# Kernel optimization log

Hardware: AMD Instinct MI355X
Metric: run time of the kernel (lower is better)

Reference implementation:

```python
import jax, jax.numpy as jnp
import numpy as np

B, H, D = 4096, 64, 32
HID, KS, K = 256, 5, 4
RES_L1_W, ENT_W, BAL_W, SPACE_W = 0.05, 0.01, 0.1, 0.1
TARGET_PROBS = jnp.array([0.5, 0.5], dtype=jnp.float32)
MIN_SPACING_RATIO = 0.5
EPS = 1e-8


def gelu(x):
    return jax.nn.gelu(x, approximate=False)  # torch nn.GELU default (exact)


def conv1d(x, w, b):
    # x: (B, Cin, H), w: (Cout, Cin, KS) -> (B, Cout, H), 'same' padding
    pad = w.shape[-1] // 2
    y = jax.lax.conv_general_dilated(
        x, w, window_strides=(1,), padding=[(pad, pad)],
        dimension_numbers=("NCH", "OIH", "NCH"))
    return y + b[None, :, None]


def _pw_linear_interp(pos, vals):
    # pos: (B, K) sorted anchor positions in [0, H-1]; vals: (B, K, D)
    t = jnp.arange(H, dtype=pos.dtype)                    # (H,)
    # index of left anchor for each timestep (searchsorted-right, K is tiny)
    idx = jnp.sum(pos[:, None, :] <= t[None, :, None], axis=-1) - 1  # (B, H)
    idx = jnp.clip(idx, 0, K - 2)
    left = jnp.take_along_axis(pos, idx, axis=1)          # (B, H)
    right = jnp.take_along_axis(pos, idx + 1, axis=1)     # (B, H)
    w = jnp.clip((t[None, :] - left) / (right - left + EPS), 0.0, 1.0)
    vl = jnp.take_along_axis(vals, idx[..., None], axis=1)        # (B, H, D)
    vr = jnp.take_along_axis(vals, (idx + 1)[..., None], axis=1)  # (B, H, D)
    return vl + w[..., None] * (vr - vl)


def setup_inputs() -> dict:
    key = jax.random.key(0)
    ks = jax.random.split(key, 24)
    s = 0.02
    inp = {
        "action_chunk": jax.random.normal(ks[0], (B, H, D), jnp.float32),
        "conv_w0": jax.random.normal(ks[1], (HID, D, KS), jnp.float32) * s,
        "conv_b0": jnp.zeros((HID,), jnp.float32),
        "conv_w1": jax.random.normal(ks[2], (HID, HID, KS), jnp.float32) * s,
        "conv_b1": jnp.zeros((HID,), jnp.float32),
        "conv_w2": jax.random.normal(ks[3], (HID, HID, KS), jnp.float32) * s,
        "conv_b2": jnp.zeros((HID,), jnp.float32),
        "proj_w": jax.random.normal(ks[4], (HID, HID), jnp.float32) * s,
        "proj_b": jnp.zeros((HID,), jnp.float32),
        "val_w1": jax.random.normal(ks[5], (HID, HID), jnp.float32) * s,
        "val_b1": jnp.zeros((HID,), jnp.float32),
        "val_w2": jax.random.normal(ks[6], (HID, K * D), jnp.float32) * s,
        "val_b2": jnp.zeros((K * D,), jnp.float32),
        "pos_w1": jax.random.normal(ks[7], (HID, HID), jnp.float32) * s,
        "pos_b1": jnp.zeros((HID,), jnp.float32),
        "pos_w2": jax.random.normal(ks[8], (HID, K), jnp.float32) * s,
        "pos_b2": jnp.zeros((K,), jnp.float32),
        "res_w1": jax.random.normal(ks[9], (HID, HID), jnp.float32) * s,
        "res_b1": jnp.zeros((HID,), jnp.float32),
        "res_w2": jax.random.normal(ks[10], (HID, H * D), jnp.float32) * s,
        "res_b2": jnp.zeros((H * D,), jnp.float32),
        "mix_w": jax.random.normal(ks[11], (HID, 2), jnp.float32) * s,
        "mix_b": jnp.zeros((2,), jnp.float32),
    }
    return inp


def reference(action_chunk, conv_w0, conv_b0, conv_w1, conv_b1, conv_w2, conv_b2,
              proj_w, proj_b, val_w1, val_b1, val_w2, val_b2,
              pos_w1, pos_b1, pos_w2, pos_b2,
              res_w1, res_b1, res_w2, res_b2, mix_w, mix_b):
    # --- temporal encoder (eval mode: dropout identity) ---
    x = jnp.swapaxes(action_chunk, 1, 2)                  # (B, D, H)
    h = gelu(conv1d(x, conv_w0, conv_b0))
    h = gelu(conv1d(h, conv_w1, conv_b1))
    h = gelu(conv1d(h, conv_w2, conv_b2))                 # (B, HID, H)
    pooled = h.mean(axis=-1)                              # adaptive avg pool -> (B, HID)
    enc = gelu(pooled @ proj_w + proj_b)                  # (B, HID)

    # --- coarse anchor decoder ---
    anchor_vals = (gelu(enc @ val_w1 + val_b1) @ val_w2 + val_b2).reshape(B, K, D)
    raw_pos = gelu(enc @ pos_w1 + pos_b1) @ pos_w2 + pos_b2          # (B, K)
    scaled = jax.nn.sigmoid(raw_pos) * float(H - 1)
    order = jnp.argsort(scaled, axis=-1)
    pos = jnp.take_along_axis(scaled, order, axis=-1)
    pos = pos.at[:, 0].set(0.0).at[:, -1].set(float(H - 1))
    vals = jnp.take_along_axis(anchor_vals, order[..., None], axis=1)
    coarse = _pw_linear_interp(pos, vals)                 # (B, H, D)

    # --- residual correction ---
    residual = (gelu(enc @ res_w1 + res_b1) @ res_w2 + res_b2).reshape(B, H, D)
    fine = coarse + residual

    # --- mixture routing (global/local) ---
    q = jax.nn.softmax(enc @ mix_w + mix_b, axis=-1)      # (B, 2)
    recon = q[:, 0, None, None] * coarse + q[:, 1, None, None] * fine

    # --- losses (fusable elementwise+reduction chain) ---
    recon_loss = jnp.mean((recon - action_chunk) ** 2)
    l1 = jnp.mean(jnp.abs(residual))
    ent = -jnp.mean(jnp.sum(q * jnp.log(q + EPS), axis=-1))
    mean_q = q.mean(axis=0)
    balance = jnp.sum((mean_q - TARGET_PROBS) ** 2)
    gaps = pos[:, 1:] - pos[:, :-1]
    min_gap = MIN_SPACING_RATIO * float(H - 1) / float(K - 1)
    spacing = jnp.mean(jnp.mean(jax.nn.relu(min_gap - gaps) ** 2, axis=-1))
    total = recon_loss + RES_L1_W * l1 + ENT_W * ent + BAL_W * balance + SPACE_W * spacing
    return total
```

## Files before the change

kernel.cpp:

```cpp
#include <hip/hip_runtime.h>

#define NB 4096

typedef __attribute__((ext_vector_type(8)))  __bf16 bf16x8;
typedef __attribute__((ext_vector_type(4)))  float  f32x4;
typedef __attribute__((ext_vector_type(16))) float  f32x16;
typedef __attribute__((ext_vector_type(8)))  int    i32x8;
typedef __attribute__((ext_vector_type(4)))  int    i32x4;

__device__ __forceinline__ float gelu_fast(float x){
    float x2 = x * x;
    float z  = x * (-1.59576912f - 0.07135482f * x2);
    float e  = __expf(z);
    return x * __builtin_amdgcn_rcpf(1.0f + e);
}
__device__ __forceinline__ unsigned short f2bf(float x){
    unsigned b = __float_as_uint(x);
    b += 0x7fffu + ((b >> 16) & 1u);
    return (unsigned short)(b >> 16);
}
__device__ __forceinline__ unsigned char f2fp8(float x){
    int p = __builtin_amdgcn_cvt_pk_fp8_f32(x, x, 0, false);
    return (unsigned char)(p & 0xff);
}
__device__ __forceinline__ unsigned f2fp4(float x){
    unsigned s = (__float_as_uint(x) >> 31) & 1u;
    float m = fabsf(x);
    int c;
    if      (m < 0.25f) c = 0;
    else if (m < 0.75f) c = 1;
    else if (m < 1.25f) c = 2;
    else if (m < 1.75f) c = 3;
    else if (m < 2.5f)  c = 4;
    else if (m < 3.5f)  c = 5;
    else if (m < 5.0f)  c = 6;
    else                c = 7;
    return (s << 3) | (unsigned)c;
}

#define O_WP0  0
#define O_WP1  40960
#define O_WP2  368640
#define O_PROJ 696320
#define O_VAL1 761856
#define O_POS1 827392
#define O_RES1 892928
#define O_VAL2 958464
#define O_RES2 991232
#define O_POS2 1515520
#define O_MIX  1519616
#define PK_TOTAL 1523712

#define WQ4_BYTES 163840

__device__ __forceinline__ unsigned short pack_std_elem(const float* W, int N, int t){
    int j = t & 7, lane = (t >> 3) & 63, rest = t >> 9;
    int ntcnt = N >> 4;
    int nt = rest % ntcnt, kk = rest / ntcnt;
    int n = nt*16 + (lane & 15), k = kk*32 + ((lane >> 4) << 3) + j;
    return f2bf(W[k * N + n]);
}
__device__ __forceinline__ unsigned short pack_pad_elem(const float* W, int Nreal, int t){
    int j = t & 7, lane = (t >> 3) & 63, kk = t >> 9;
    int n = lane & 15, k = kk*32 + ((lane >> 4) << 3) + j;
    return (n < Nreal) ? f2bf(W[k * Nreal + n]) : (unsigned short)0;
}
__device__ __forceinline__ unsigned char pack_fp4_byte(const float* W, int t){
    int byt = t & 15, lane = (t >> 4) & 63, g = (t >> 10) & 7, S = t >> 13;
    int n = g*32 + (lane & 31);
    int kbase = S*64 + ((lane >> 5) << 5) + (byt << 1);
    int k0 = kbase, k1 = kbase + 1;
    float v0 = W[n*1280 + (k0 & 255)*5 + (k0 >> 8)] * 64.0f;
    float v1 = W[n*1280 + (k1 & 255)*5 + (k1 >> 8)] * 64.0f;
    return (unsigned char)(f2fp4(v0) | (f2fp4(v1) << 4));
}

__global__ __launch_bounds__(256) void pack_weights(
    const float* __restrict__ W0, const float* __restrict__ W1, const float* __restrict__ W2,
    const float* __restrict__ proj_w, const float* __restrict__ val_w1,
    const float* __restrict__ pos_w1, const float* __restrict__ res_w1,
    const float* __restrict__ val_w2, const float* __restrict__ res_w2,
    const float* __restrict__ pos_w2, const float* __restrict__ mix_w,
    unsigned short* __restrict__ pk,
    unsigned char* __restrict__ wq1, unsigned char* __restrict__ wq2)
{
    int idx = blockIdx.x * 256 + threadIdx.x;
    if (idx >= PK_TOTAL) return;
    if (idx < O_WP1){
        int t = idx;
        int j = t & 7, lane = (t >> 3) & 63, nt = (t >> 9) & 7, s = t >> 12;
        int co = nt*32 + (lane & 31);
        int tap = s >> 1, ci = ((s & 1) << 4) + ((lane >> 5) << 3) + j;
        pk[idx] = f2bf(W0[co*160 + ci*5 + tap]);
    } else if (idx < O_WP1 + WQ4_BYTES){
        wq1[idx - O_WP1] = pack_fp4_byte(W1, idx - O_WP1);
    } else if (idx < O_WP2){
    } else if (idx < O_WP2 + WQ4_BYTES){
        wq2[idx - O_WP2] = pack_fp4_byte(W2, idx - O_WP2);
    } else if (idx < O_PROJ){
    }
    else if (idx < O_VAL1) pk[idx] = pack_std_elem(proj_w, 256, idx - O_PROJ);
    else if (idx < O_POS1) pk[idx] = pack_std_elem(val_w1, 256, idx - O_VAL1);
    else if (idx < O_RES1) pk[idx] = pack_std_elem(pos_w1, 256, idx - O_POS1);
    else if (idx < O_VAL2) pk[idx] = pack_std_elem(res_w1, 256, idx - O_RES1);
    else if (idx < O_RES2) pk[idx] = pack_std_elem(val_w2, 128, idx - O_VAL2);
    else if (idx < O_POS2) pk[idx] = pack_std_elem(res_w2, 2048, idx - O_RES2);
    else if (idx < O_MIX)  pk[idx] = pack_pad_elem(pos_w2, 4, idx - O_POS2);
    else                   pk[idx] = pack_pad_elem(mix_w, 2, idx - O_MIX);
}

#define HT_P 272
#define XT_S 40
#define INV512 0.001953125f
#define SCALE1 0x7F

__global__ __launch_bounds__(256, 4) void conv_mfma_kernel(
    const float* __restrict__ A,
    const float* __restrict__ B0, const float* __restrict__ B1, const float* __restrict__ B2,
    const unsigned short* __restrict__ wp0,
    const unsigned char* __restrict__ wq1, const unsigned char* __restrict__ wq2,
    unsigned short* __restrict__ pooled)
{
    __shared__ __align__(16) unsigned short xt[68 * XT_S];
    __shared__ __align__(16) unsigned char  ht8[68 * HT_P];

    const int tid  = threadIdx.x;
    const int b    = blockIdx.x;
    const int w    = tid >> 6;
    const int lane = tid & 63;
    const int l31  = lane & 31;
    const int hi   = lane >> 5;
    const int hi8  = hi << 3;
    const int w64  = w << 6;

    for (int i = tid; i < 4 * HT_P; i += 256){
        int r = i / HT_P, c = i - r * HT_P;
        int rr = (r < 2 ? r : r + 64);
        ht8[rr * HT_P + c] = 0;
    }
    if (tid < 128){
        int r = tid >> 5, c = tid & 31;
        int rr = (r < 2 ? r : r + 64);
        xt[rr * XT_S + c] = 0;
    }
    {
        const float* Ab = A + (size_t)b * 2048;
        int e0 = tid << 3;
        int t = e0 >> 5, c = e0 & 31;
        const float4* p = (const float4*)(Ab + e0);
        float4 v0 = p[0], v1 = p[1];
        union { unsigned short u[8]; bf16x8 v; } pkv;
        pkv.u[0]=f2bf(v0.x); pkv.u[1]=f2bf(v0.y); pkv.u[2]=f2bf(v0.z); pkv.u[3]=f2bf(v0.w);
        pkv.u[4]=f2bf(v1.x); pkv.u[5]=f2bf(v1.y); pkv.u[6]=f2bf(v1.z); pkv.u[7]=f2bf(v1.w);
        *(bf16x8*)&xt[(t + 2) * XT_S + c] = pkv.v;
    }
    __syncthreads();

    f32x16 acc[2][2];

#define ZEROALL \
    { _Pragma("unroll") for (int mt = 0; mt < 2; ++mt) \
      _Pragma("unroll") for (int nn = 0; nn < 2; ++nn) \
      _Pragma("unroll") for (int r = 0; r < 16; ++r) acc[mt][nn][r] = 0.f; }

#define LOADAX(BUF, S) \
    { _Pragma("unroll") for (int mt = 0; mt < 2; ++mt) \
          BUF[mt] = *(const bf16x8*)&xt[((mt << 5) + l31 + ((S) >> 1)) * XT_S + (((S) & 1) << 4) + hi8]; }
#define LOADB0(BUF, S) \
    { _Pragma("unroll") for (int nn = 0; nn < 2; ++nn) \
          BUF[nn] = *(const bf16x8*)(b0ptr + nn * 512 + (S) * 4096); }
#define MFX(X_, B_) \
    { _Pragma("unroll") for (int mt = 0; mt < 2; ++mt) \
      _Pragma("unroll") for (int nn = 0; nn < 2; ++nn) \
          acc[mt][nn] = __builtin_amdgcn_mfma_f32_32x32x16_bf16(X_[mt], B_[nn], acc[mt][nn], 0, 0, 0); }

#define LOADA_MX(DST, S) \
    { _Pragma("unroll") for (int mt = 0; mt < 2; ++mt) \
          DST[mt] = *(const i32x8*)&ht8[((mt << 5) + l31 + ((S) >> 2)) * HT_P + (((S) & 3) << 6) + (hi << 5)]; }
#define LOADB4(DST, S, BPTR) \
    { _Pragma("unroll") for (int nn = 0; nn < 2; ++nn) \
          *(i32x4*)&DST[nn] = *(const i32x4*)((BPTR) + (size_t)(S) * 8192 + nn * 1024); }
#define MFMX4(A_, B_) \
    { _Pragma("unroll") for (int mt = 0; mt < 2; ++mt) \
      _Pragma("unroll") for (int nn = 0; nn < 2; ++nn) \
          acc[mt][nn] = __builtin_amdgcn_mfma_scale_f32_32x32x64_f8f6f4( \
              A_[mt], B_[nn], acc[mt][nn], 0, 4, 0, SCALE1, 0, SCALE1); }

#define EPI_C0(BIAS) \
    { float bvn[2]; \
      _Pragma("unroll") for (int nn = 0; nn < 2; ++nn) bvn[nn] = (BIAS)[w64 + (nn << 5) + l31]; \
      _Pragma("unroll") for (int mt = 0; mt < 2; ++mt) \
      _Pragma("unroll") for (int nn = 0; nn < 2; ++nn) \
      _Pragma("unroll") for (int r = 0; r < 16; ++r){ \
          int row = (mt << 5) + (r & 3) + ((r >> 2) << 3) + (hi << 2) + 2; \
          float v = gelu_fast(acc[mt][nn][r] + bvn[nn]); \
          ht8[row * HT_P + w64 + (nn << 5) + l31] = f2fp8(v * 8.0f); } }

#define EPI_MX(BIAS) \
    { float bvn[2]; \
      _Pragma("unroll") for (int nn = 0; nn < 2; ++nn) bvn[nn] = (BIAS)[w64 + (nn << 5) + l31]; \
      _Pragma("unroll") for (int mt = 0; mt < 2; ++mt) \
      _Pragma("unroll") for (int nn = 0; nn < 2; ++nn) \
      _Pragma("unroll") for (int r = 0; r < 16; ++r){ \
          int row = (mt << 5) + (r & 3) + ((r >> 2) << 3) + (hi << 2) + 2; \
          float v = gelu_fast(acc[mt][nn][r] * INV512 + bvn[nn]); \
          ht8[row * HT_P + w64 + (nn << 5) + l31] = f2fp8(v * 8.0f); } }

#define CONV_MX4(WQ) \
    { const unsigned char* bptr = (WQ) + (size_t)((w << 11) + lane * 16); \
      i32x8 Bf[2][2]; i32x8 Af[2][2]; \
      _Pragma("unroll") for (int rr_ = 0; rr_ < 2; ++rr_) \
      _Pragma("unroll") for (int nn = 0; nn < 2; ++nn) \
      _Pragma("unroll") for (int e_ = 0; e_ < 8; ++e_) Bf[rr_][nn][e_] = 0; \
      LOADB4(Bf[0], 0, bptr); LOADA_MX(Af[0], 0); \
      LOADB4(Bf[1], 1, bptr); LOADA_MX(Af[1], 1); \
      _Pragma("unroll") \
      for (int s = 0; s < 20; ++s){ \
          MFMX4(Af[s & 1], Bf[s & 1]); \
          if (s + 2 < 20){ LOADB4(Bf[s & 1], s + 2, bptr); LOADA_MX(Af[s & 1], s + 2); } \
      } }

    ZEROALL;
    {
        const unsigned short* b0ptr = wp0 + (size_t)((w << 10) + lane * 8);
        bf16x8 Bc[2][2]; bf16x8 Xc[2][2];
        LOADB0(Bc[0], 0); LOADAX(Xc[0], 0);
        LOADB0(Bc[1], 1); LOADAX(Xc[1], 1);
        #pragma unroll
        for (int s = 0; s < 10; ++s){
            MFX(Xc[s & 1], Bc[s & 1]);
            if (s + 2 < 10){ LOADB0(Bc[s & 1], s + 2); LOADAX(Xc[s & 1], s + 2); }
        }
    }
    EPI_C0(B0);
    __syncthreads();

    ZEROALL;
    CONV_MX4(wq1);
    __syncthreads();
    EPI_MX(B1);
    __syncthreads();

    ZEROALL;
    CONV_MX4(wq2);
    {
        float bvn[2];
        #pragma unroll
        for (int nn = 0; nn < 2; ++nn) bvn[nn] = B2[w64 + (nn << 5) + l31];
        #pragma unroll
        for (int nn = 0; nn < 2; ++nn){
            float a = 0.f;
            #pragma unroll
            for (int mt = 0; mt < 2; ++mt)
                #pragma unroll
                for (int r = 0; r < 16; ++r)
                    a += gelu_fast(acc[mt][nn][r] * INV512 + bvn[nn]);
            a += __shfl_xor(a, 32);
            if (hi == 0)
                pooled[(size_t)b * 256 + w64 + (nn << 5) + l31] = f2bf(a * (1.0f / 64.0f));
        }
    }
}

#define AS 264

__global__ __launch_bounds__(256) void heads_a_kernel(
    const unsigned short* __restrict__ pooled,
    const float* __restrict__ proj_b, const float* __restrict__ val_b1,
    const float* __restrict__ pos_b1, const float* __restrict__ res_b1,
    const float* __restrict__ val_b2, const float* __restrict__ pos_b2,
    const float* __restrict__ mix_b,
    const unsigned short* __restrict__ pk,
    unsigned short* __restrict__ rh, float* __restrict__ meta,
    float* __restrict__ accums)
{
    __shared__ unsigned short pb [16 * AS];
    __shared__ unsigned short eb [16 * AS];
    __shared__ unsigned short vb [16 * AS];
    __shared__ unsigned short phb[16 * AS];
    __shared__ unsigned short rhb[16 * AS];
    __shared__ float av [16 * 132];
    __shared__ float avs[16 * 132];
    __shared__ float psort[16][4];
    __shared__ int   rank [16][4];
    __shared__ float qsh  [16][2];
    __shared__ float mlsh [16][2];
    __shared__ float sposh[16][4];

    const int tid  = threadIdx.x;
    const int b0   = blockIdx.x * 16;
    const int w    = tid >> 6;
    const int lane = tid & 63;
    const int l15  = lane & 15;
    const int q    = lane >> 4;
    const int q8   = q << 3;
    const int q4   = q << 2;

    {
        int g = tid >> 4, seg = tid & 15;
        const unsigned short* ps = pooled + ((size_t)(b0 + g) << 8) + (seg << 4);
        bf16x8 a0 = *(const bf16x8*)ps;
        bf16x8 a1 = *(const bf16x8*)(ps + 8);
        *(bf16x8*)&pb[g * AS + (seg << 4)]     = a0;
        *(bf16x8*)&pb[g * AS + (seg << 4) + 8] = a1;
    }
    __syncthreads();

#define HGEMM256(ASRC, GOFF, BIAS, DST) \
    { f32x4 hacc[4]; \
      _Pragma("unroll") for (int nt = 0; nt < 4; ++nt) hacc[nt] = (f32x4){0.f,0.f,0.f,0.f}; \
      _Pragma("unroll") for (int kk = 0; kk < 8; ++kk){ \
          bf16x8 af = *(const bf16x8*)&(ASRC)[l15 * AS + (kk << 5) + q8]; \
          _Pragma("unroll") for (int nt = 0; nt < 4; ++nt){ \
              bf16x8 bfr = *(const bf16x8*)(pk + (GOFF) + (size_t)((((kk << 4) + (w << 2) + nt) << 6) + lane) * 8); \
              hacc[nt] = __builtin_amdgcn_mfma_f32_16x16x32_bf16(af, bfr, hacc[nt], 0, 0, 0); } } \
      _Pragma("unroll") for (int nt = 0; nt < 4; ++nt){ \
          int n = (w << 6) + (nt << 4) + l15; \
          float bv = (BIAS)[n]; \
          _Pragma("unroll") for (int r = 0; r < 4; ++r) \
              (DST)[(q4 + r) * AS + n] = f2bf(gelu_fast(hacc[nt][r] + bv)); } }

    HGEMM256(pb, O_PROJ, proj_b, eb);
    __syncthreads();

    HGEMM256(eb, O_VAL1, val_b1, vb);
    HGEMM256(eb, O_POS1, pos_b1, phb);
    HGEMM256(eb, O_RES1, res_b1, rhb);
    __syncthreads();

    {
        f32x4 acc2[2];
        #pragma unroll
        for (int nt = 0; nt < 2; ++nt) acc2[nt] = (f32x4){0.f,0.f,0.f,0.f};
        #pragma unroll
        for (int kk = 0; kk < 8; ++kk){
            bf16x8 af = *(const bf16x8*)&vb[l15 * AS + (kk << 5) + q8];
            #pragma unroll
            for (int nt = 0; nt < 2; ++nt){
                bf16x8 bfr = *(const bf16x8*)(pk + O_VAL2 + (size_t)(((kk*8 + w*2 + nt) << 6) + lane) * 8);
                acc2[nt] = __builtin_amdgcn_mfma_f32_16x16x32_bf16(af, bfr, acc2[nt], 0, 0, 0);
            }
        }
        #pragma unroll
        for (int nt = 0; nt < 2; ++nt){
            int j = (w << 5) + (nt << 4) + l15;
            float bv = val_b2[j];
            #pragma unroll
            for (int r = 0; r < 4; ++r)
                av[(q4 + r) * 132 + j] = acc2[nt][r] + bv;
        }
    }
    if (w == 0){
        f32x4 accp = (f32x4){0.f,0.f,0.f,0.f};
        #pragma unroll
        for (int kk = 0; kk < 8; ++kk){
            bf16x8 af  = *(const bf16x8*)&phb[l15 * AS + (kk << 5) + q8];
            bf16x8 bfr = *(const bf16x8*)(pk + O_POS2 + (size_t)((kk << 6) + lane) * 8);
            accp = __builtin_amdgcn_mfma_f32_16x16x32_bf16(af, bfr, accp, 0, 0, 0);
        }
        if (l15 < 4){
            float bv = pos_b2[l15];
            #pragma unroll
            for (int r = 0; r < 4; ++r){
                float raw = accp[r] + bv;
                sposh[q4 + r][l15] = 63.0f * __builtin_amdgcn_rcpf(1.0f + __expf(-raw));
            }
        }
    } else if (w == 1){
        f32x4 accm = (f32x4){0.f,0.f,0.f,0.f};
        #pragma unroll
        for (int kk = 0; kk < 8; ++kk){
            bf16x8 af  = *(const bf16x8*)&eb[l15 * AS + (kk << 5) + q8];
            bf16x8 bfr = *(const bf16x8*)(pk + O_MIX + (size_t)((kk << 6) + lane) * 8);
            accm = __builtin_amdgcn_mfma_f32_16x16x32_bf16(af, bfr, accm, 0, 0, 0);
        }
        if (l15 < 2){
            #pragma unroll
            for (int r = 0; r < 4; ++r)
                mlsh[q4 + r][l15] = accm[r] + mix_b[l15];
        }
    }
    __syncthreads();

    if (tid < 16){
        int g = tid;
        float sv[4] = { sposh[g][0], sposh[g][1], sposh[g][2], sposh[g][3] };
        #pragma unroll
        for (int i = 0; i < 4; ++i){
            int r = 0;
            #pragma unroll
            for (int jj = 0; jj < 4; ++jj){
                r += (sv[jj] < sv[i]) ? 1 : 0;
                if (jj < i) r += (sv[jj] == sv[i]) ? 1 : 0;
            }
            rank[g][i] = r;
            psort[g][r] = sv[i];
        }
        psort[g][0] = 0.0f; psort[g][3] = 63.0f;
        float p1 = psort[g][1], p2 = psort[g][2];
        float g1 = p1, g2 = p2 - p1, g3 = 63.0f - p2;
        const float MG = 10.5f;
        float r1 = fmaxf(MG - g1, 0.f), r2 = fmaxf(MG - g2, 0.f), r3 = fmaxf(MG - g3, 0.f);
        float sp = (r1*r1 + r2*r2 + r3*r3) * (1.0f / 3.0f);
        float l0 = mlsh[g][0], l1 = mlsh[g][1];
        float m = fmaxf(l0, l1);
        float e0 = __expf(l0 - m), e1 = __expf(l1 - m);
        float inv = 1.0f / (e0 + e1);
        float q0 = e0 * inv, q1 = e1 * inv;
        qsh[g][0] = q0; qsh[g][1] = q1;
        float entc = q0 * logf(q0 + 1e-8f) + q1 * logf(q1 + 1e-8f);
        atomicAdd(&accums[2], entc);
        atomicAdd(&accums[3], q0);
        atomicAdd(&accums[4], q1);
        atomicAdd(&accums[5], sp);
    }
    __syncthreads();

    #pragma unroll
    for (int u2 = 0; u2 < 8; ++u2){
        int idx2 = tid * 8 + u2;
        int g = idx2 >> 7, j = idx2 & 127;
        avs[g * 132 + rank[g][j >> 5] * 32 + (j & 31)] = av[g * 132 + j];
    }
    __syncthreads();

    {
        int g = tid >> 4, c16 = (tid & 15) << 4;
        bf16x8 a0 = *(const bf16x8*)&rhb[g * AS + c16];
        bf16x8 a1 = *(const bf16x8*)&rhb[g * AS + c16 + 8];
        unsigned short* dst = rh + ((size_t)(b0 + g) << 8) + c16;
        *(bf16x8*)dst       = a0;
        *(bf16x8*)(dst + 8) = a1;
    }
    if (tid < 132){
        for (int g = 0; g < 16; ++g){
            float v;
            if (tid < 128)       v = avs[g * 132 + tid];
            else if (tid == 128) v = psort[g][1];
            else if (tid == 129) v = psort[g][2];
            else if (tid == 130) v = qsh[g][0];
            else                 v = qsh[g][1];
            meta[(size_t)(b0 + g) * 132 + tid] = v;
        }
    }
}

__global__ __launch_bounds__(256) void resid_loss_kernel(
    const float* __restrict__ A, const unsigned short* __restrict__ rh,
    const float* __restrict__ res_b2, const unsigned short* __restrict__ pk,
    const float* __restrict__ meta, float* __restrict__ accums)
{
    __shared__ float ml[16 * 132];
    __shared__ float wred[4], wred2[4];

    const int tid  = threadIdx.x;
    const int w    = tid >> 6;
    const int lane = tid & 63;
    const int l15  = lane & 15;
    const int q    = lane >> 4;
    const int q8   = q << 3;
    const int q4   = q << 2;
    const int bg   = blockIdx.x >> 2;
    const int cc   = blockIdx.x & 3;
    const int b0   = bg << 4;

    for (int i = tid; i < 16 * 132; i += 256)
        ml[i] = meta[(size_t)b0 * 132 + i];
    __syncthreads();

    f32x4 acc[8];
    #pragma unroll
    for (int nt = 0; nt < 8; ++nt) acc[nt] = (f32x4){0.f,0.f,0.f,0.f};
    #pragma unroll
    for (int kk = 0; kk < 8; ++kk){
        bf16x8 af = *(const bf16x8*)(rh + ((size_t)(b0 + l15) << 8) + (kk << 5) + q8);
        #pragma unroll
        for (int nt = 0; nt < 8; ++nt){
            int ntg = (cc << 5) + (w << 3) + nt;
            bf16x8 bfr = *(const bf16x8*)(pk + O_RES2 + (size_t)((kk << 7) + ntg) * 512 + (lane << 3));
            acc[nt] = __builtin_amdgcn_mfma_f32_16x16x32_bf16(af, bfr, acc[nt], 0, 0, 0);
        }
    }

    float lsq = 0.f, ll1 = 0.f;
    #pragma unroll
    for (int nt = 0; nt < 8; ++nt){
        int e = (cc << 9) + (w << 7) + (nt << 4) + l15;
        float rbv = res_b2[e];
        int t = e >> 5, d = e & 31;
        float tf = (float)t;
        #pragma unroll
        for (int r = 0; r < 4; ++r){
            int g = q4 + r;
            const float* mg = &ml[g * 132];
            float p1 = mg[128], p2 = mg[129], q0 = mg[130], q1 = mg[131];
            float res = acc[nt][r] + rbv;
            int cnt = (p1 <= tf) + (p2 <= tf) + (tf >= 63.0f);
            int idx = cnt < 2 ? cnt : 2;
            float left  = idx == 0 ? 0.0f : (idx == 1 ? p1 : p2);
            float right = idx == 0 ? p1   : (idx == 1 ? p2 : 63.0f);
            float wgt = (tf - left) / (right - left + 1e-8f);
            wgt = fminf(fmaxf(wgt, 0.f), 1.f);
            float vl = mg[idx * 32 + d];
            float vr = mg[idx * 32 + 32 + d];
            float coarse = vl + wgt * (vr - vl);
            float a = A[((size_t)(b0 + g) << 11) + e];
            float fine = coarse + res;
            float recon = q0 * coarse + q1 * fine;
            float dd = recon - a;
            lsq += dd * dd;
            ll1 += fabsf(res);
        }
    }
    #pragma unroll
    for (int off = 32; off > 0; off >>= 1){
        lsq += __shfl_down(lsq, off);
        ll1 += __shfl_down(ll1, off);
    }
    if (lane == 0){ wred[w] = lsq; wred2[w] = ll1; }
    __syncthreads();
    if (tid == 0){
        atomicAdd(&accums[0], wred[0] + wred[1] + wred[2] + wred[3]);
        atomicAdd(&accums[1], wred2[0] + wred2[1] + wred2[2] + wred2[3]);
    }
}

__global__ void finalize_kernel(const float* __restrict__ accums, float* __restrict__ out){
    float rs = accums[0], l1s = accums[1], ents = accums[2];
    float q0s = accums[3], q1s = accums[4], sps = accums[5];
    const float invN = 1.0f / (4096.0f * 2048.0f);
    const float invB = 1.0f / 4096.0f;
    float recon_loss = rs * invN;
    float l1   = l1s * invN;
    float ent  = -ents * invB;
    float mq0  = q0s * invB - 0.5f, mq1 = q1s * invB - 0.5f;
    float balance = mq0*mq0 + mq1*mq1;
    float spacing = sps * invB;
    out[0] = recon_loss + 0.05f*l1 + 0.01f*ent + 0.1f*balance + 0.1f*spacing;
}

extern "C" void kernel_launch(void* const* d_in, const int* in_sizes, int n_in,
                              void* d_out, int out_size, void* d_ws, size_t ws_size,
                              hipStream_t stream)
{
    const float* A      = (const float*)d_in[0];
    const float* W0     = (const float*)d_in[1];
    const float* B0     = (const float*)d_in[2];
    const float* W1     = (const float*)d_in[3];
    const float* B1     = (const float*)d_in[4];
    const float* W2     = (const float*)d_in[5];
    const float* B2     = (const float*)d_in[6];
    const float* proj_w = (const float*)d_in[7];
    const float* proj_b = (const float*)d_in[8];
    const float* val_w1 = (const float*)d_in[9];
    const float* val_b1 = (const float*)d_in[10];
    const float* val_w2 = (const float*)d_in[11];
    const float* val_b2 = (const float*)d_in[12];
    const float* pos_w1 = (const float*)d_in[13];
    const float* pos_b1 = (const float*)d_in[14];
    const float* pos_w2 = (const float*)d_in[15];
    const float* pos_b2 = (const float*)d_in[16];
    const float* res_w1 = (const float*)d_in[17];
    const float* res_b1 = (const float*)d_in[18];
    const float* res_w2 = (const float*)d_in[19];
    const float* res_b2 = (const float*)d_in[20];
    const float* mix_w  = (const float*)d_in[21];
    const float* mix_b  = (const float*)d_in[22];

    char* wsb = (char*)d_ws;
    float* accums = (float*)wsb;
    unsigned short* pooled = (unsigned short*)(wsb + 256);
    unsigned short* pkbuf  = (unsigned short*)(wsb + 256 + 2097152);
    unsigned short* rhbuf  = (unsigned short*)(wsb + 256 + 2097152 + (size_t)PK_TOTAL * 2);
    float* metabuf = (float*)(wsb + 256 + 2097152 + (size_t)PK_TOTAL * 2 + 2097152);
    unsigned char* wq1 = (unsigned char*)(wsb + 256 + 2097152 + (size_t)PK_TOTAL * 2 + 2097152
                                          + (size_t)4096 * 132 * 4);
    unsigned char* wq2 = wq1 + WQ4_BYTES;

    hipMemsetAsync(accums, 0, 64 * sizeof(float), stream);

    hipLaunchKernelGGL(pack_weights, dim3((PK_TOTAL + 255) / 256), dim3(256), 0, stream,
                       W0, W1, W2, proj_w, val_w1, pos_w1, res_w1,
                       val_w2, res_w2, pos_w2, mix_w, pkbuf, wq1, wq2);

    hipLaunchKernelGGL(conv_mfma_kernel, dim3(NB), dim3(256), 0, stream,
                       A, B0, B1, B2,
                       pkbuf + O_WP0, wq1, wq2, pooled);

    hipLaunchKernelGGL(heads_a_kernel, dim3(NB / 16), dim3(256), 0, stream,
                       pooled, proj_b, val_b1, pos_b1, res_b1, val_b2, pos_b2, mix_b,
                       pkbuf, rhbuf, metabuf, accums);

    hipLaunchKernelGGL(resid_loss_kernel, dim3(NB / 16 * 4), dim3(256), 0, stream,
                       A, rhbuf, res_b2, pkbuf, metabuf, accums);

    hipLaunchKernelGGL(finalize_kernel, dim3(1), dim3(1), 0, stream,
                       accums, (float*)d_out);
}
```

Measured before the change: 378.5 us.

## Double heads kernel block to 512 threads and redistribute GEMM work across eight waves

The heads kernel now launches 512 threads (8 waves) per 16-row group instead of 256. The proj GEMM is split over 8 waves, the three hidden GEMMs (val/pos/res) are each split across a pair of waves, and the mix head runs on a spare wave concurrently with them. The val2 and pos2 heads move to separate waves so they run in parallel. The aim is more wave-level parallelism in a kernel with only 256 blocks, at the cost of more registers per wave (8 accumulators) and lower occupancy per CU.

```diff
diff --git a/kernel.cpp b/kernel.cpp
--- a/kernel.cpp
+++ b/kernel.cpp
@@ -264,7 +264,7 @@
 
 #define AS 264
 
-__global__ __launch_bounds__(256) void heads_a_kernel(
+__global__ __launch_bounds__(512) void heads_a_kernel(
     const unsigned short* __restrict__ pooled,
     const float* __restrict__ proj_b, const float* __restrict__ val_b1,
     const float* __restrict__ pos_b1, const float* __restrict__ res_b1,
@@ -296,7 +296,7 @@
     const int q8   = q << 3;
     const int q4   = q << 2;
 
-    {
+    if (tid < 256){
         int g = tid >> 4, seg = tid & 15;
         const unsigned short* ps = pooled + ((size_t)(b0 + g) << 8) + (seg << 4);
         bf16x8 a0 = *(const bf16x8*)ps;
@@ -306,29 +306,72 @@
     }
     __syncthreads();
 
-#define HGEMM256(ASRC, GOFF, BIAS, DST) \
-    { f32x4 hacc[4]; \
-      _Pragma("unroll") for (int nt = 0; nt < 4; ++nt) hacc[nt] = (f32x4){0.f,0.f,0.f,0.f}; \
-      _Pragma("unroll") for (int kk = 0; kk < 8; ++kk){ \
-          bf16x8 af = *(const bf16x8*)&(ASRC)[l15 * AS + (kk << 5) + q8]; \
-          _Pragma("unroll") for (int nt = 0; nt < 4; ++nt){ \
-              bf16x8 bfr = *(const bf16x8*)(pk + (GOFF) + (size_t)((((kk << 4) + (w << 2) + nt) << 6) + lane) * 8); \
-              hacc[nt] = __builtin_amdgcn_mfma_f32_16x16x32_bf16(af, bfr, hacc[nt], 0, 0, 0); } } \
-      _Pragma("unroll") for (int nt = 0; nt < 4; ++nt){ \
-          int n = (w << 6) + (nt << 4) + l15; \
-          float bv = (BIAS)[n]; \
-          _Pragma("unroll") for (int r = 0; r < 4; ++r) \
-              (DST)[(q4 + r) * AS + n] = f2bf(gelu_fast(hacc[nt][r] + bv)); } }
-
-    HGEMM256(pb, O_PROJ, proj_b, eb);
-    __syncthreads();
-
-    HGEMM256(eb, O_VAL1, val_b1, vb);
-    HGEMM256(eb, O_POS1, pos_b1, phb);
-    HGEMM256(eb, O_RES1, res_b1, rhb);
-    __syncthreads();
-
     {
+        f32x4 hacc[2];
+        #pragma unroll
+        for (int nt = 0; nt < 2; ++nt) hacc[nt] = (f32x4){0.f,0.f,0.f,0.f};
+        #pragma unroll
+        for (int kk = 0; kk < 8; ++kk){
+            bf16x8 af = *(const bf16x8*)&pb[l15 * AS + (kk << 5) + q8];
+            #pragma unroll
+            for (int nt = 0; nt < 2; ++nt){
+                bf16x8 bfr = *(const bf16x8*)(pk + O_PROJ + (size_t)((((kk << 4) + (w << 1) + nt) << 6) + lane) * 8);
+                hacc[nt] = __builtin_amdgcn_mfma_f32_16x16x32_bf16(af, bfr, hacc[nt], 0, 0, 0);
+            }
+        }
+        #pragma unroll
+        for (int nt = 0; nt < 2; ++nt){
+            int n = (w << 5) + (nt << 4) + l15;
+            float bv = proj_b[n];
+            #pragma unroll
+            for (int r = 0; r < 4; ++r)
+                eb[(q4 + r) * AS + n] = f2bf(gelu_fast(hacc[nt][r] + bv));
+        }
+    }
+    __syncthreads();
+
+    if (w < 6){
+        const int pair = w >> 1, half = w & 1;
+        const int goff = (pair == 0) ? O_VAL1 : (pair == 1) ? O_POS1 : O_RES1;
+        const float* bias = (pair == 0) ? val_b1 : (pair == 1) ? pos_b1 : res_b1;
+        unsigned short* dst = (pair == 0) ? vb : (pair == 1) ? phb : rhb;
+        f32x4 hacc[8];
+        #pragma unroll
+        for (int nt = 0; nt < 8; ++nt) hacc[nt] = (f32x4){0.f,0.f,0.f,0.f};
+        #pragma unroll
+        for (int kk = 0; kk < 8; ++kk){
+            bf16x8 af = *(const bf16x8*)&eb[l15 * AS + (kk << 5) + q8];
+            #pragma unroll
+            for (int nt = 0; nt < 8; ++nt){
+                bf16x8 bfr = *(const bf16x8*)(pk + goff + (size_t)((((kk << 4) + (half << 3) + nt) << 6) + lane) * 8);
+                hacc[nt] = __builtin_amdgcn_mfma_f32_16x16x32_bf16(af, bfr, hacc[nt], 0, 0, 0);
+            }
+        }
+        #pragma unroll
+        for (int nt = 0; nt < 8; ++nt){
+            int n = (half << 7) + (nt << 4) + l15;
+            float bv = bias[n];
+            #pragma unroll
+            for (int r = 0; r < 4; ++r)
+                dst[(q4 + r) * AS + n] = f2bf(gelu_fast(hacc[nt][r] + bv));
+        }
+    } else if (w == 6){
+        f32x4 accm = (f32x4){0.f,0.f,0.f,0.f};
+        #pragma unroll
+        for (int kk = 0; kk < 8; ++kk){
+            bf16x8 af  = *(const bf16x8*)&eb[l15 * AS + (kk << 5) + q8];
+            bf16x8 bfr = *(const bf16x8*)(pk + O_MIX + (size_t)((kk << 6) + lane) * 8);
+            accm = __builtin_amdgcn_mfma_f32_16x16x32_bf16(af, bfr, accm, 0, 0, 0);
+        }
+        if (l15 < 2){
+            #pragma unroll
+            for (int r = 0; r < 4; ++r)
+                mlsh[q4 + r][l15] = accm[r] + mix_b[l15];
+        }
+    }
+    __syncthreads();
+
+    if (w < 4){
         f32x4 acc2[2];
         #pragma unroll
         for (int nt = 0; nt < 2; ++nt) acc2[nt] = (f32x4){0.f,0.f,0.f,0.f};
@@ -349,8 +392,7 @@
             for (int r = 0; r < 4; ++r)
                 av[(q4 + r) * 132 + j] = acc2[nt][r] + bv;
         }
-    }
-    if (w == 0){
+    } else if (w == 4){
         f32x4 accp = (f32x4){0.f,0.f,0.f,0.f};
         #pragma unroll
         for (int kk = 0; kk < 8; ++kk){
@@ -365,19 +407,6 @@
                 float raw = accp[r] + bv;
                 sposh[q4 + r][l15] = 63.0f * __builtin_amdgcn_rcpf(1.0f + __expf(-raw));
             }
-        }
-    } else if (w == 1){
-        f32x4 accm = (f32x4){0.f,0.f,0.f,0.f};
-        #pragma unroll
-        for (int kk = 0; kk < 8; ++kk){
-            bf16x8 af  = *(const bf16x8*)&eb[l15 * AS + (kk << 5) + q8];
-            bf16x8 bfr = *(const bf16x8*)(pk + O_MIX + (size_t)((kk << 6) + lane) * 8);
-            accm = __builtin_amdgcn_mfma_f32_16x16x32_bf16(af, bfr, accm, 0, 0, 0);
-        }
-        if (l15 < 2){
-            #pragma unroll
-            for (int r = 0; r < 4; ++r)
-                mlsh[q4 + r][l15] = accm[r] + mix_b[l15];
         }
     }
     __syncthreads();
@@ -417,14 +446,14 @@
     __syncthreads();
 
     #pragma unroll
-    for (int u2 = 0; u2 < 8; ++u2){
-        int idx2 = tid * 8 + u2;
+    for (int u2 = 0; u2 < 4; ++u2){
+        int idx2 = tid * 4 + u2;
         int g = idx2 >> 7, j = idx2 & 127;
         avs[g * 132 + rank[g][j >> 5] * 32 + (j & 31)] = av[g * 132 + j];
     }
     __syncthreads();
 
-    {
+    if (tid < 256){
         int g = tid >> 4, c16 = (tid & 15) << 4;
         bf16x8 a0 = *(const bf16x8*)&rhb[g * AS + c16];
         bf16x8 a1 = *(const bf16x8*)&rhb[g * AS + c16 + 8];
@@ -587,7 +616,7 @@
                        A, B0, B1, B2,
                        pkbuf + O_WP0, wq1, wq2, pooled);
 
-    hipLaunchKernelGGL(heads_a_kernel, dim3(NB / 16), dim3(256), 0, stream,
+    hipLaunchKernelGGL(heads_a_kernel, dim3(NB / 16), dim3(512), 0, stream,
                        pooled, proj_b, val_b1, pos_b1, res_b1, val_b2, pos_b2, mix_b,
                        pkbuf, rhbuf, metabuf, accums);
 
```

Result: faster. 348.9 us (median of 2 runs) (-7.8%).
